# Performance work log

Hardware: AMD Instinct MI355X
Metric: run time of the kernel (lower is better)

## Reference

```python
import jax, jax.numpy as jnp
import numpy as np

NH, DK, DV = 8, 10, 10  # num_heads, per-head key dim, per-head value dim (dim_k=dim_v=80)


def setup_inputs() -> dict:
    key = jax.random.key(0)
    k1, k2, k3, k4, k5 = jax.random.split(key, 5)
    B, NX, NY = 64, 512, 512
    x = jax.random.normal(k1, (B, NX, 768), dtype=jnp.float32)
    y = jax.random.normal(k2, (B, NY, 283), dtype=jnp.float32)
    # nn.Linear(bias=False) weights, stored transposed as (in, out); scaled init
    Wq = jax.random.normal(k3, (768, 80), dtype=jnp.float32) * 0.02
    Wk = jax.random.normal(k4, (283, 80), dtype=jnp.float32) * 0.02
    Wv = jax.random.normal(k5, (283, 80), dtype=jnp.float32) * 0.02
    return {"x": x, "y": y, "Wq": Wq, "Wk": Wk, "Wv": Wv}


def reference(x, y, Wq, Wk, Wv):
    B, nx, _ = x.shape
    ny = y.shape[1]
    # projections -> split heads: (B, nh, seq, dhead)
    q = (x @ Wq).reshape(B, nx, NH, DK).transpose(0, 2, 1, 3)
    k = (y @ Wk).reshape(B, ny, NH, DK).transpose(0, 2, 1, 3)
    v = (y @ Wv).reshape(B, ny, NH, DV).transpose(0, 2, 1, 3)
    scale = 1.0 / np.sqrt(DK).astype(np.float32)
    dist = jax.nn.softmax(jnp.einsum("bhqd,bhkd->bhqk", q, k) * scale, axis=-1)
    att = q + jnp.einsum("bhqk,bhkd->bhqd", dist, v)  # residual add of q
    att = att.transpose(0, 2, 1, 3).reshape(B, nx, NH * DV)
    # module returns `result` = flattened attention (fc/BN stack is dead code)
    return att.reshape(B, -1)
```

## Files before the change

### kernel.cpp

```cpp
#include <hip/hip_runtime.h>
#include <stdint.h>

typedef unsigned short u16;
typedef unsigned int   u32;
typedef _Float16       f16;

typedef __attribute__((ext_vector_type(2))) _Float16 half2v;
typedef __attribute__((ext_vector_type(4))) _Float16 half4v;
typedef __attribute__((ext_vector_type(8))) _Float16 half8v;
typedef __attribute__((ext_vector_type(4))) float    floatx4;

#define NXS    512
#define NYS    512
#define NHEAD  8
#define DHEAD  10
#define DMODEL 80
#define DXK    768
#define DYK    283

__device__ inline half2v pk2(float x, float y) {
  return __builtin_bit_cast(half2v, __builtin_amdgcn_cvt_pkrtz(x, y));
}
__device__ inline half4v cvt4(float4 v) {
  return __builtin_shufflevector(pk2(v.x, v.y), pk2(v.z, v.w), 0, 1, 2, 3);
}

__global__ __launch_bounds__(256) void w_prep(const float* __restrict__ Wq,
                                              const float* __restrict__ Wk,
                                              const float* __restrict__ Wv,
                                              f16* __restrict__ Tq,
                                              f16* __restrict__ Tk,
                                              f16* __restrict__ Tv) {
  const int idx = blockIdx.x * 256 + threadIdx.x;
  if (idx < 80 * 768) {
    const int c = idx / 768, k = idx - c * 768;
    Tq[idx] = (f16)Wq[k * 80 + c];
  }
  if (idx < 80 * 288) {
    const int c = idx / 288, k = idx - c * 288;
    float a = 0.f, b = 0.f;
    if (k < DYK) { a = Wk[k * 80 + c]; b = Wv[k * 80 + c]; }
    Tk[idx] = (f16)a;
    Tv[idx] = (f16)b;
  }
}

__global__ __launch_bounds__(256) void proj_q(const float* __restrict__ X,
                                              const f16* __restrict__ Wt,
                                              f16* __restrict__ O) {
  __shared__ f16 Xs[64 * 40];
  __shared__ f16 Ws[80 * 40];
  const int t = threadIdx.x;
  const int wv = t >> 6, lane = t & 63, m16 = lane & 15, quad = lane >> 4;
  const int row0 = blockIdx.x * 64;
  const int xr_r = t >> 3, xr_k = (t & 7) << 2;
  const int wi0 = t, wi1 = t + 160;

  float4 xr0, xr1;
  uint4 wr0, wr1;
  xr0 = *(const float4*)&X[(size_t)(row0 + xr_r) * DXK + xr_k];
  xr1 = *(const float4*)&X[(size_t)(row0 + xr_r + 32) * DXK + xr_k];
  if (t < 160) {
    wr0 = *(const uint4*)&Wt[(wi0 >> 2) * DXK + (wi0 & 3) * 8];
    wr1 = *(const uint4*)&Wt[(wi1 >> 2) * DXK + (wi1 & 3) * 8];
  }

  floatx4 acc[5];
#pragma unroll
  for (int i = 0; i < 5; ++i) acc[i] = (floatx4){0.f, 0.f, 0.f, 0.f};

  for (int s = 0; s < 24; ++s) {
    if (s) __syncthreads();
    *(half4v*)&Xs[xr_r * 40 + xr_k] = cvt4(xr0);
    *(half4v*)&Xs[(xr_r + 32) * 40 + xr_k] = cvt4(xr1);
    if (t < 160) {
      *(uint4*)&Ws[(wi0 >> 2) * 40 + (wi0 & 3) * 8] = wr0;
      *(uint4*)&Ws[(wi1 >> 2) * 40 + (wi1 & 3) * 8] = wr1;
    }
    __syncthreads();
    if (s < 23) {
      const int k0 = (s + 1) * 32;
      xr0 = *(const float4*)&X[(size_t)(row0 + xr_r) * DXK + k0 + xr_k];
      xr1 = *(const float4*)&X[(size_t)(row0 + xr_r + 32) * DXK + k0 + xr_k];
      if (t < 160) {
        wr0 = *(const uint4*)&Wt[(wi0 >> 2) * DXK + k0 + (wi0 & 3) * 8];
        wr1 = *(const uint4*)&Wt[(wi1 >> 2) * DXK + k0 + (wi1 & 3) * 8];
      }
    }
    const half8v a = *(const half8v*)&Xs[(wv * 16 + m16) * 40 + quad * 8];
#pragma unroll
    for (int nt = 0; nt < 5; ++nt) {
      const half8v b = *(const half8v*)&Ws[(nt * 16 + m16) * 40 + quad * 8];
      acc[nt] = __builtin_amdgcn_mfma_f32_16x16x32_f16(a, b, acc[nt], 0, 0, 0);
    }
  }
#pragma unroll
  for (int nt = 0; nt < 5; ++nt) {
    const int col = nt * 16 + m16;
#pragma unroll
    for (int p = 0; p < 4; ++p) {
      const int grow = row0 + wv * 16 + quad * 4 + p;
      O[(size_t)grow * DMODEL + col] = (f16)acc[nt][p];
    }
  }
}

__global__ __launch_bounds__(256) void proj_kv(const float* __restrict__ Y,
                                               const f16* __restrict__ Wtk,
                                               const f16* __restrict__ Wtv,
                                               f16* __restrict__ Ko,
                                               f16* __restrict__ Vo) {
  __shared__ f16 Ys[64 * 40];
  __shared__ f16 Wks[80 * 40];
  __shared__ f16 Wvs[80 * 40];
  const int t = threadIdx.x;
  const int wv = t >> 6, lane = t & 63, m16 = lane & 15, quad = lane >> 4;
  const int row0 = blockIdx.x * 64;
  const int wi0 = t, wi1 = t + 160;

  float yr[8];
  uint4 wk0, wk1, wv0, wv1;
#pragma unroll
  for (int i = 0; i < 8; ++i) {
    const int idx = t + 256 * i;
    const int r = idx >> 5, kk = idx & 31;
    yr[i] = (kk < DYK) ? Y[(size_t)(row0 + r) * DYK + kk] : 0.f;
  }
  if (t < 160) {
    wk0 = *(const uint4*)&Wtk[(wi0 >> 2) * 288 + (wi0 & 3) * 8];
    wk1 = *(const uint4*)&Wtk[(wi1 >> 2) * 288 + (wi1 & 3) * 8];
    wv0 = *(const uint4*)&Wtv[(wi0 >> 2) * 288 + (wi0 & 3) * 8];
    wv1 = *(const uint4*)&Wtv[(wi1 >> 2) * 288 + (wi1 & 3) * 8];
  }

  floatx4 ak[5], av[5];
#pragma unroll
  for (int i = 0; i < 5; ++i) {
    ak[i] = (floatx4){0.f, 0.f, 0.f, 0.f};
    av[i] = (floatx4){0.f, 0.f, 0.f, 0.f};
  }

  for (int s = 0; s < 9; ++s) {
    if (s) __syncthreads();
#pragma unroll
    for (int i = 0; i < 8; ++i) {
      const int idx = t + 256 * i;
      Ys[(idx >> 5) * 40 + (idx & 31)] = (f16)yr[i];
    }
    if (t < 160) {
      *(uint4*)&Wks[(wi0 >> 2) * 40 + (wi0 & 3) * 8] = wk0;
      *(uint4*)&Wks[(wi1 >> 2) * 40 + (wi1 & 3) * 8] = wk1;
      *(uint4*)&Wvs[(wi0 >> 2) * 40 + (wi0 & 3) * 8] = wv0;
      *(uint4*)&Wvs[(wi1 >> 2) * 40 + (wi1 & 3) * 8] = wv1;
    }
    __syncthreads();
    if (s < 8) {
      const int k0 = (s + 1) * 32;
#pragma unroll
      for (int i = 0; i < 8; ++i) {
        const int idx = t + 256 * i;
        const int r = idx >> 5, k = k0 + (idx & 31);
        yr[i] = (k < DYK) ? Y[(size_t)(row0 + r) * DYK + k] : 0.f;
      }
      if (t < 160) {
        wk0 = *(const uint4*)&Wtk[(wi0 >> 2) * 288 + k0 + (wi0 & 3) * 8];
        wk1 = *(const uint4*)&Wtk[(wi1 >> 2) * 288 + k0 + (wi1 & 3) * 8];
        wv0 = *(const uint4*)&Wtv[(wi0 >> 2) * 288 + k0 + (wi0 & 3) * 8];
        wv1 = *(const uint4*)&Wtv[(wi1 >> 2) * 288 + k0 + (wi1 & 3) * 8];
      }
    }
    const half8v a = *(const half8v*)&Ys[(wv * 16 + m16) * 40 + quad * 8];
#pragma unroll
    for (int nt = 0; nt < 5; ++nt) {
      const half8v bk = *(const half8v*)&Wks[(nt * 16 + m16) * 40 + quad * 8];
      ak[nt] = __builtin_amdgcn_mfma_f32_16x16x32_f16(a, bk, ak[nt], 0, 0, 0);
      const half8v bv = *(const half8v*)&Wvs[(nt * 16 + m16) * 40 + quad * 8];
      av[nt] = __builtin_amdgcn_mfma_f32_16x16x32_f16(a, bv, av[nt], 0, 0, 0);
    }
  }
#pragma unroll
  for (int nt = 0; nt < 5; ++nt) {
    const int col = nt * 16 + m16;
    const int h = col / 10, d = col - h * 10;
#pragma unroll
    for (int p = 0; p < 4; ++p) {
      const int grow = row0 + wv * 16 + quad * 4 + p;
      const int bb = grow >> 9, ny = grow & 511;
      const size_t o = (((size_t)bb * NHEAD + h) * NYS + ny) * DHEAD + d;
      Ko[o] = (f16)ak[nt][p];
      Vo[o] = (f16)av[nt][p];
    }
  }
}

__global__ __launch_bounds__(256) void attn(const f16* __restrict__ Q,
                                            const f16* __restrict__ K,
                                            const f16* __restrict__ V,
                                            float* __restrict__ O) {
  __shared__ f16 Qs[512 * 20];
  __shared__ f16 Ks[512 * 20];
  __shared__ f16 Vt[16 * 520];
  const int t = threadIdx.x;
  const int wv = t >> 6, lane = t & 63, m16 = lane & 15, quad = lane >> 4;
  const int b = blockIdx.x >> 3, h = blockIdx.x & 7;

  u32* Qs32 = (u32*)Qs;
  u32* Ks32 = (u32*)Ks;
  u32* Vt32 = (u32*)Vt;
  const u32* Qg = (const u32*)Q + (size_t)b * NXS * 40 + h * 5;
  const u32* Kg = (const u32*)K + (size_t)(b * NHEAD + h) * NYS * 5;
  const u32* Vg = (const u32*)V + (size_t)(b * NHEAD + h) * NYS * 5;

  for (int idx = t; idx < 2560; idx += 256) {
    const u32 row = (u32)idx / 5u, c = (u32)idx - row * 5u;
    Qs32[row * 10 + c] = Qg[row * 40 + c];
    Ks32[row * 10 + c] = Kg[idx];
    const half2v hv = __builtin_bit_cast(half2v, Vg[idx]);
    Vt[(2 * c) * 520 + row] = hv[0];
    Vt[(2 * c + 1) * 520 + row] = hv[1];
  }
  for (int idx = t; idx < 2560; idx += 256) {
    const u32 row = (u32)idx / 5u, c = 5u + ((u32)idx - row * 5u);
    Qs32[row * 10 + c] = 0u;
    Ks32[row * 10 + c] = 0u;
  }
  for (int idx = t; idx < 1560; idx += 256) {
    Vt32[2600 + idx] = 0u;
  }
  __syncthreads();

  const float scale = 0.31622776601683794f;
#pragma unroll 1
  for (int i = 0; i < 8; ++i) {
    const int qt = wv * 8 + i;
    const half4v qf = *(const half4v*)&Qs[(qt * 16 + m16) * 20 + quad * 4];
    floatx4 oacc = (floatx4){0.f, 0.f, 0.f, 0.f};
    float lp = 0.f;
    for (int kt = 0; kt < 32; ++kt) {
      const half4v kf = *(const half4v*)&Ks[(kt * 16 + m16) * 20 + quad * 4];
      floatx4 s = __builtin_amdgcn_mfma_f32_16x16x16f16(kf, qf,
                    (floatx4){0.f, 0.f, 0.f, 0.f}, 0, 0, 0);
      const float p0 = __expf(s[0] * scale);
      const float p1 = __expf(s[1] * scale);
      const float p2 = __expf(s[2] * scale);
      const float p3 = __expf(s[3] * scale);
      lp += (p0 + p1) + (p2 + p3);
      const half4v pf = __builtin_shufflevector(pk2(p0, p1), pk2(p2, p3), 0, 1, 2, 3);
      const half4v vf = *(const half4v*)&Vt[m16 * 520 + kt * 16 + quad * 4];
      oacc = __builtin_amdgcn_mfma_f32_16x16x16f16(pf, vf, oacc, 0, 0, 0);
    }
    lp += __shfl_xor(lp, 16);
    lp += __shfl_xor(lp, 32);
#pragma unroll
    for (int p = 0; p < 4; ++p) {
      const int rq = qt * 16 + quad * 4 + p;
      const float lr = __shfl(lp, quad * 4 + p);
      const float qv = (float)Qs[rq * 20 + m16];
      const float val = qv + oacc[p] / lr;
      if (m16 < DHEAD)
        O[((size_t)b * NXS + rq) * DMODEL + h * DHEAD + m16] = val;
    }
  }
}

extern "C" void kernel_launch(void* const* d_in, const int* in_sizes, int n_in,
                              void* d_out, int out_size, void* d_ws, size_t ws_size,
                              hipStream_t stream) {
  const float* x  = (const float*)d_in[0];
  const float* y  = (const float*)d_in[1];
  const float* Wq = (const float*)d_in[2];
  const float* Wk = (const float*)d_in[3];
  const float* Wv = (const float*)d_in[4];
  float* out = (float*)d_out;

  char* ws = (char*)d_ws;
  f16* Wtq = (f16*)(ws);
  f16* Wtk = (f16*)(ws + 122880);
  f16* Wtv = (f16*)(ws + 168960);
  f16* Qw  = (f16*)(ws + 262144);
  f16* Kw  = (f16*)(ws + 5505024);
  f16* Vw  = (f16*)(ws + 10747904);

  w_prep <<<240, 256, 0, stream>>>(Wq, Wk, Wv, Wtq, Wtk, Wtv);
  proj_q <<<512, 256, 0, stream>>>(x, Wtq, Qw);
  proj_kv<<<512, 256, 0, stream>>>(y, Wtk, Wtv, Kw, Vw);
  attn   <<<512, 256, 0, stream>>>(Qw, Kw, Vw, out);
}
```

Measured before the change: 238.3 us.

## Merge projection kernels, drop LDS staging, split attention blocks by query half

The Q and K/V projection kernels are merged into one launch of 1024 blocks. Each wave now loads X/Y rows and weight fragments straight from global memory into MFMA operands, with no shared-memory staging and no barriers. The attention kernel is split into two blocks per (batch, head), reads Q fragments directly from global memory, folds the scale into Q, uses padded LDS strides, and keeps two accumulators to split the dependency chain. The trade is more redundant global/L2 traffic for the weights in exchange for more parallelism and fewer syncs, and K/V tiles are now staged twice per head.

```diff
diff --git a/kernel.cpp b/kernel.cpp
--- a/kernel.cpp
+++ b/kernel.cpp
@@ -17,12 +17,17 @@
 #define DMODEL 80
 #define DXK    768
 #define DYK    283
+#define DYKP   288
 
 __device__ inline half2v pk2(float x, float y) {
   return __builtin_bit_cast(half2v, __builtin_amdgcn_cvt_pkrtz(x, y));
 }
 __device__ inline half4v cvt4(float4 v) {
   return __builtin_shufflevector(pk2(v.x, v.y), pk2(v.z, v.w), 0, 1, 2, 3);
+}
+__device__ inline half4v h4u32(u32 a, u32 b) {
+  return __builtin_shufflevector(__builtin_bit_cast(half2v, a),
+                                 __builtin_bit_cast(half2v, b), 0, 1, 2, 3);
 }
 
 __global__ __launch_bounds__(256) void w_prep(const float* __restrict__ Wq,
@@ -45,150 +50,97 @@
   }
 }
 
-__global__ __launch_bounds__(256) void proj_q(const float* __restrict__ X,
-                                              const f16* __restrict__ Wt,
-                                              f16* __restrict__ O) {
-  __shared__ f16 Xs[64 * 40];
-  __shared__ f16 Ws[80 * 40];
+__global__ __launch_bounds__(256) void proj(const float* __restrict__ X,
+                                            const float* __restrict__ Y,
+                                            const f16* __restrict__ Wtq,
+                                            const f16* __restrict__ Wtk,
+                                            const f16* __restrict__ Wtv,
+                                            f16* __restrict__ Qw,
+                                            f16* __restrict__ Kw,
+                                            f16* __restrict__ Vw) {
   const int t = threadIdx.x;
   const int wv = t >> 6, lane = t & 63, m16 = lane & 15, quad = lane >> 4;
-  const int row0 = blockIdx.x * 64;
-  const int xr_r = t >> 3, xr_k = (t & 7) << 2;
-  const int wi0 = t, wi1 = t + 160;
-
-  float4 xr0, xr1;
-  uint4 wr0, wr1;
-  xr0 = *(const float4*)&X[(size_t)(row0 + xr_r) * DXK + xr_k];
-  xr1 = *(const float4*)&X[(size_t)(row0 + xr_r + 32) * DXK + xr_k];
-  if (t < 160) {
-    wr0 = *(const uint4*)&Wt[(wi0 >> 2) * DXK + (wi0 & 3) * 8];
-    wr1 = *(const uint4*)&Wt[(wi1 >> 2) * DXK + (wi1 & 3) * 8];
-  }
-
-  floatx4 acc[5];
-#pragma unroll
-  for (int i = 0; i < 5; ++i) acc[i] = (floatx4){0.f, 0.f, 0.f, 0.f};
-
-  for (int s = 0; s < 24; ++s) {
-    if (s) __syncthreads();
-    *(half4v*)&Xs[xr_r * 40 + xr_k] = cvt4(xr0);
-    *(half4v*)&Xs[(xr_r + 32) * 40 + xr_k] = cvt4(xr1);
-    if (t < 160) {
-      *(uint4*)&Ws[(wi0 >> 2) * 40 + (wi0 & 3) * 8] = wr0;
-      *(uint4*)&Ws[(wi1 >> 2) * 40 + (wi1 & 3) * 8] = wr1;
-    }
-    __syncthreads();
-    if (s < 23) {
-      const int k0 = (s + 1) * 32;
-      xr0 = *(const float4*)&X[(size_t)(row0 + xr_r) * DXK + k0 + xr_k];
-      xr1 = *(const float4*)&X[(size_t)(row0 + xr_r + 32) * DXK + k0 + xr_k];
-      if (t < 160) {
-        wr0 = *(const uint4*)&Wt[(wi0 >> 2) * DXK + k0 + (wi0 & 3) * 8];
-        wr1 = *(const uint4*)&Wt[(wi1 >> 2) * DXK + k0 + (wi1 & 3) * 8];
-      }
-    }
-    const half8v a = *(const half8v*)&Xs[(wv * 16 + m16) * 40 + quad * 8];
+  const int blk = blockIdx.x;
+
+  if (blk < 512) {
+    const int rowb = blk * 64 + wv * 16;
+    const float* xr = X + (size_t)(rowb + m16) * DXK + quad * 8;
+    const f16* wb = Wtq + (size_t)m16 * DXK + quad * 8;
+
+    floatx4 acc[5];
+#pragma unroll
+    for (int i = 0; i < 5; ++i) acc[i] = (floatx4){0.f, 0.f, 0.f, 0.f};
+
+#pragma unroll 4
+    for (int s = 0; s < 24; ++s) {
+      const int k0 = s * 32;
+      const float4 x0 = *(const float4*)(xr + k0);
+      const float4 x1 = *(const float4*)(xr + k0 + 4);
+      const half8v a = __builtin_shufflevector(cvt4(x0), cvt4(x1),
+                                               0, 1, 2, 3, 4, 5, 6, 7);
+#pragma unroll
+      for (int nt = 0; nt < 5; ++nt) {
+        const half8v b = *(const half8v*)(wb + (size_t)nt * 16 * DXK + k0);
+        acc[nt] = __builtin_amdgcn_mfma_f32_16x16x32_f16(a, b, acc[nt], 0, 0, 0);
+      }
+    }
 #pragma unroll
     for (int nt = 0; nt < 5; ++nt) {
-      const half8v b = *(const half8v*)&Ws[(nt * 16 + m16) * 40 + quad * 8];
-      acc[nt] = __builtin_amdgcn_mfma_f32_16x16x32_f16(a, b, acc[nt], 0, 0, 0);
-    }
-  }
-#pragma unroll
-  for (int nt = 0; nt < 5; ++nt) {
-    const int col = nt * 16 + m16;
-#pragma unroll
-    for (int p = 0; p < 4; ++p) {
-      const int grow = row0 + wv * 16 + quad * 4 + p;
-      O[(size_t)grow * DMODEL + col] = (f16)acc[nt][p];
-    }
-  }
-}
-
-__global__ __launch_bounds__(256) void proj_kv(const float* __restrict__ Y,
-                                               const f16* __restrict__ Wtk,
-                                               const f16* __restrict__ Wtv,
-                                               f16* __restrict__ Ko,
-                                               f16* __restrict__ Vo) {
-  __shared__ f16 Ys[64 * 40];
-  __shared__ f16 Wks[80 * 40];
-  __shared__ f16 Wvs[80 * 40];
-  const int t = threadIdx.x;
-  const int wv = t >> 6, lane = t & 63, m16 = lane & 15, quad = lane >> 4;
-  const int row0 = blockIdx.x * 64;
-  const int wi0 = t, wi1 = t + 160;
-
-  float yr[8];
-  uint4 wk0, wk1, wv0, wv1;
-#pragma unroll
-  for (int i = 0; i < 8; ++i) {
-    const int idx = t + 256 * i;
-    const int r = idx >> 5, kk = idx & 31;
-    yr[i] = (kk < DYK) ? Y[(size_t)(row0 + r) * DYK + kk] : 0.f;
-  }
-  if (t < 160) {
-    wk0 = *(const uint4*)&Wtk[(wi0 >> 2) * 288 + (wi0 & 3) * 8];
-    wk1 = *(const uint4*)&Wtk[(wi1 >> 2) * 288 + (wi1 & 3) * 8];
-    wv0 = *(const uint4*)&Wtv[(wi0 >> 2) * 288 + (wi0 & 3) * 8];
-    wv1 = *(const uint4*)&Wtv[(wi1 >> 2) * 288 + (wi1 & 3) * 8];
-  }
-
-  floatx4 ak[5], av[5];
-#pragma unroll
-  for (int i = 0; i < 5; ++i) {
-    ak[i] = (floatx4){0.f, 0.f, 0.f, 0.f};
-    av[i] = (floatx4){0.f, 0.f, 0.f, 0.f};
-  }
-
-  for (int s = 0; s < 9; ++s) {
-    if (s) __syncthreads();
-#pragma unroll
-    for (int i = 0; i < 8; ++i) {
-      const int idx = t + 256 * i;
-      Ys[(idx >> 5) * 40 + (idx & 31)] = (f16)yr[i];
-    }
-    if (t < 160) {
-      *(uint4*)&Wks[(wi0 >> 2) * 40 + (wi0 & 3) * 8] = wk0;
-      *(uint4*)&Wks[(wi1 >> 2) * 40 + (wi1 & 3) * 8] = wk1;
-      *(uint4*)&Wvs[(wi0 >> 2) * 40 + (wi0 & 3) * 8] = wv0;
-      *(uint4*)&Wvs[(wi1 >> 2) * 40 + (wi1 & 3) * 8] = wv1;
-    }
-    __syncthreads();
-    if (s < 8) {
-      const int k0 = (s + 1) * 32;
-#pragma unroll
-      for (int i = 0; i < 8; ++i) {
-        const int idx = t + 256 * i;
-        const int r = idx >> 5, k = k0 + (idx & 31);
-        yr[i] = (k < DYK) ? Y[(size_t)(row0 + r) * DYK + k] : 0.f;
-      }
-      if (t < 160) {
-        wk0 = *(const uint4*)&Wtk[(wi0 >> 2) * 288 + k0 + (wi0 & 3) * 8];
-        wk1 = *(const uint4*)&Wtk[(wi1 >> 2) * 288 + k0 + (wi1 & 3) * 8];
-        wv0 = *(const uint4*)&Wtv[(wi0 >> 2) * 288 + k0 + (wi0 & 3) * 8];
-        wv1 = *(const uint4*)&Wtv[(wi1 >> 2) * 288 + k0 + (wi1 & 3) * 8];
-      }
-    }
-    const half8v a = *(const half8v*)&Ys[(wv * 16 + m16) * 40 + quad * 8];
+      const int col = nt * 16 + m16;
+#pragma unroll
+      for (int p = 0; p < 4; ++p)
+        Qw[(size_t)(rowb + quad * 4 + p) * DMODEL + col] = (f16)acc[nt][p];
+    }
+  } else {
+    const int rowb = (blk - 512) * 64 + wv * 16;
+    const float* yr = Y + (size_t)(rowb + m16) * DYK + quad * 8;
+    const f16* wbk = Wtk + (size_t)m16 * DYKP + quad * 8;
+    const f16* wbv = Wtv + (size_t)m16 * DYKP + quad * 8;
+
+    floatx4 ak[5], av[5];
+#pragma unroll
+    for (int i = 0; i < 5; ++i) {
+      ak[i] = (floatx4){0.f, 0.f, 0.f, 0.f};
+      av[i] = (floatx4){0.f, 0.f, 0.f, 0.f};
+    }
+
+#pragma unroll 2
+    for (int s = 0; s < 9; ++s) {
+      const int k0 = s * 32;
+      float y8[8];
+      if (s < 8) {
+#pragma unroll
+        for (int j = 0; j < 8; ++j) y8[j] = yr[k0 + j];
+      } else {
+#pragma unroll
+        for (int j = 0; j < 8; ++j) {
+          const int k = k0 + quad * 8 + j;
+          y8[j] = (k < DYK) ? yr[k0 + j] : 0.f;
+        }
+      }
+      const half8v a = __builtin_shufflevector(
+          cvt4((float4){y8[0], y8[1], y8[2], y8[3]}),
+          cvt4((float4){y8[4], y8[5], y8[6], y8[7]}), 0, 1, 2, 3, 4, 5, 6, 7);
+#pragma unroll
+      for (int nt = 0; nt < 5; ++nt) {
+        const half8v bk = *(const half8v*)(wbk + (size_t)nt * 16 * DYKP + k0);
+        ak[nt] = __builtin_amdgcn_mfma_f32_16x16x32_f16(a, bk, ak[nt], 0, 0, 0);
+        const half8v bv = *(const half8v*)(wbv + (size_t)nt * 16 * DYKP + k0);
+        av[nt] = __builtin_amdgcn_mfma_f32_16x16x32_f16(a, bv, av[nt], 0, 0, 0);
+      }
+    }
 #pragma unroll
     for (int nt = 0; nt < 5; ++nt) {
-      const half8v bk = *(const half8v*)&Wks[(nt * 16 + m16) * 40 + quad * 8];
-      ak[nt] = __builtin_amdgcn_mfma_f32_16x16x32_f16(a, bk, ak[nt], 0, 0, 0);
-      const half8v bv = *(const half8v*)&Wvs[(nt * 16 + m16) * 40 + quad * 8];
-      av[nt] = __builtin_amdgcn_mfma_f32_16x16x32_f16(a, bv, av[nt], 0, 0, 0);
-    }
-  }
-#pragma unroll
-  for (int nt = 0; nt < 5; ++nt) {
-    const int col = nt * 16 + m16;
-    const int h = col / 10, d = col - h * 10;
-#pragma unroll
-    for (int p = 0; p < 4; ++p) {
-      const int grow = row0 + wv * 16 + quad * 4 + p;
-      const int bb = grow >> 9, ny = grow & 511;
-      const size_t o = (((size_t)bb * NHEAD + h) * NYS + ny) * DHEAD + d;
-      Ko[o] = (f16)ak[nt][p];
-      Vo[o] = (f16)av[nt][p];
+      const int col = nt * 16 + m16;
+      const int h = col / 10, d = col - h * 10;
+#pragma unroll
+      for (int p = 0; p < 4; ++p) {
+        const int grow = rowb + quad * 4 + p;
+        const int bb = grow >> 9, ny = grow & 511;
+        const size_t o = (((size_t)bb * NHEAD + h) * NYS + ny) * DHEAD + d;
+        Kw[o] = (f16)ak[nt][p];
+        Vw[o] = (f16)av[nt][p];
+      }
     }
   }
 }
@@ -197,68 +149,92 @@
                                             const f16* __restrict__ K,
                                             const f16* __restrict__ V,
                                             float* __restrict__ O) {
-  __shared__ f16 Qs[512 * 20];
-  __shared__ f16 Ks[512 * 20];
-  __shared__ f16 Vt[16 * 520];
+  __shared__ f16 Ks[512 * 22];
+  __shared__ f16 Vt[16 * 522];
   const int t = threadIdx.x;
   const int wv = t >> 6, lane = t & 63, m16 = lane & 15, quad = lane >> 4;
-  const int b = blockIdx.x >> 3, h = blockIdx.x & 7;
-
-  u32* Qs32 = (u32*)Qs;
-  u32* Ks32 = (u32*)Ks;
-  u32* Vt32 = (u32*)Vt;
-  const u32* Qg = (const u32*)Q + (size_t)b * NXS * 40 + h * 5;
-  const u32* Kg = (const u32*)K + (size_t)(b * NHEAD + h) * NYS * 5;
-  const u32* Vg = (const u32*)V + (size_t)(b * NHEAD + h) * NYS * 5;
-
+  const int bh = blockIdx.x >> 1, half = blockIdx.x & 1;
+  const int b = bh >> 3, h = bh & 7;
+
+  const u32* Kg = (const u32*)K + (size_t)bh * NYS * 5;
+  const u32* Vg = (const u32*)V + (size_t)bh * NYS * 5;
   for (int idx = t; idx < 2560; idx += 256) {
     const u32 row = (u32)idx / 5u, c = (u32)idx - row * 5u;
-    Qs32[row * 10 + c] = Qg[row * 40 + c];
-    Ks32[row * 10 + c] = Kg[idx];
-    const half2v hv = __builtin_bit_cast(half2v, Vg[idx]);
-    Vt[(2 * c) * 520 + row] = hv[0];
-    Vt[(2 * c + 1) * 520 + row] = hv[1];
-  }
-  for (int idx = t; idx < 2560; idx += 256) {
-    const u32 row = (u32)idx / 5u, c = 5u + ((u32)idx - row * 5u);
-    Qs32[row * 10 + c] = 0u;
-    Ks32[row * 10 + c] = 0u;
-  }
-  for (int idx = t; idx < 1560; idx += 256) {
-    Vt32[2600 + idx] = 0u;
-  }
+    const half2v kv = __builtin_bit_cast(half2v, Kg[idx]);
+    Ks[row * 22 + 2 * c]     = kv[0];
+    Ks[row * 22 + 2 * c + 1] = kv[1];
+    const half2v vv = __builtin_bit_cast(half2v, Vg[idx]);
+    Vt[(2 * c) * 522 + row]     = vv[0];
+    Vt[(2 * c + 1) * 522 + row] = vv[1];
+  }
+  for (int idx = t; idx < 3072; idx += 256) {
+    const u32 row = (u32)idx / 6u, d = 10u + ((u32)idx - row * 6u);
+    Ks[row * 22 + d] = (f16)0.f;
+  }
+  for (int idx = t; idx < 6 * 522; idx += 256)
+    Vt[10 * 522 + idx] = (f16)0.f;
   __syncthreads();
 
   const float scale = 0.31622776601683794f;
 #pragma unroll 1
-  for (int i = 0; i < 8; ++i) {
-    const int qt = wv * 8 + i;
-    const half4v qf = *(const half4v*)&Qs[(qt * 16 + m16) * 20 + quad * 4];
-    floatx4 oacc = (floatx4){0.f, 0.f, 0.f, 0.f};
-    float lp = 0.f;
-    for (int kt = 0; kt < 32; ++kt) {
-      const half4v kf = *(const half4v*)&Ks[(kt * 16 + m16) * 20 + quad * 4];
-      floatx4 s = __builtin_amdgcn_mfma_f32_16x16x16f16(kf, qf,
-                    (floatx4){0.f, 0.f, 0.f, 0.f}, 0, 0, 0);
-      const float p0 = __expf(s[0] * scale);
-      const float p1 = __expf(s[1] * scale);
-      const float p2 = __expf(s[2] * scale);
-      const float p3 = __expf(s[3] * scale);
-      lp += (p0 + p1) + (p2 + p3);
-      const half4v pf = __builtin_shufflevector(pk2(p0, p1), pk2(p2, p3), 0, 1, 2, 3);
-      const half4v vf = *(const half4v*)&Vt[m16 * 520 + kt * 16 + quad * 4];
-      oacc = __builtin_amdgcn_mfma_f32_16x16x16f16(pf, vf, oacc, 0, 0, 0);
-    }
+  for (int i = 0; i < 4; ++i) {
+    const int qt = half * 16 + wv * 4 + i;
+    const int qrow = qt * 16 + m16;
+    const u32* Qg32 = (const u32*)(Q + ((size_t)b * NXS + qrow) * DMODEL + h * DHEAD);
+    float s0 = 0.f, s1 = 0.f, s2 = 0.f, s3 = 0.f;
+    if (quad < 2) {
+      const u32 ua = Qg32[quad * 2], ub = Qg32[quad * 2 + 1];
+      const half2v ha = __builtin_bit_cast(half2v, ua);
+      const half2v hb = __builtin_bit_cast(half2v, ub);
+      s0 = (float)ha[0]; s1 = (float)ha[1]; s2 = (float)hb[0]; s3 = (float)hb[1];
+    } else if (quad == 2) {
+      const u32 ua = Qg32[4];
+      const half2v ha = __builtin_bit_cast(half2v, ua);
+      s0 = (float)ha[0]; s1 = (float)ha[1];
+    }
+    const half4v qf = __builtin_shufflevector(pk2(s0 * scale, s1 * scale),
+                                              pk2(s2 * scale, s3 * scale),
+                                              0, 1, 2, 3);
+    floatx4 o0 = (floatx4){0.f, 0.f, 0.f, 0.f};
+    floatx4 o1 = (floatx4){0.f, 0.f, 0.f, 0.f};
+    float l0 = 0.f, l1 = 0.f;
+    for (int kt = 0; kt < 32; kt += 2) {
+#pragma unroll
+      for (int u = 0; u < 2; ++u) {
+        const int ktu = kt + u;
+        const int kb = (ktu * 16 + m16) * 22 + quad * 4;
+        const half4v kf = h4u32(*(const u32*)&Ks[kb], *(const u32*)&Ks[kb + 2]);
+        const floatx4 s = __builtin_amdgcn_mfma_f32_16x16x16f16(
+            kf, qf, (floatx4){0.f, 0.f, 0.f, 0.f}, 0, 0, 0);
+        const float p0 = __expf(s[0]);
+        const float p1 = __expf(s[1]);
+        const float p2 = __expf(s[2]);
+        const float p3 = __expf(s[3]);
+        const half4v pf = __builtin_shufflevector(pk2(p0, p1), pk2(p2, p3),
+                                                  0, 1, 2, 3);
+        const int vb = m16 * 522 + ktu * 16 + quad * 4;
+        const half4v vf = h4u32(*(const u32*)&Vt[vb], *(const u32*)&Vt[vb + 2]);
+        if (u == 0) {
+          l0 += (p0 + p1) + (p2 + p3);
+          o0 = __builtin_amdgcn_mfma_f32_16x16x16f16(pf, vf, o0, 0, 0, 0);
+        } else {
+          l1 += (p0 + p1) + (p2 + p3);
+          o1 = __builtin_amdgcn_mfma_f32_16x16x16f16(pf, vf, o1, 0, 0, 0);
+        }
+      }
+    }
+    float lp = l0 + l1;
     lp += __shfl_xor(lp, 16);
     lp += __shfl_xor(lp, 32);
 #pragma unroll
     for (int p = 0; p < 4; ++p) {
       const int rq = qt * 16 + quad * 4 + p;
       const float lr = __shfl(lp, quad * 4 + p);
-      const float qv = (float)Qs[rq * 20 + m16];
-      const float val = qv + oacc[p] / lr;
-      if (m16 < DHEAD)
-        O[((size_t)b * NXS + rq) * DMODEL + h * DHEAD + m16] = val;
+      if (m16 < DHEAD) {
+        const float qres = (float)Q[((size_t)b * NXS + rq) * DMODEL + h * DHEAD + m16];
+        O[((size_t)b * NXS + rq) * DMODEL + h * DHEAD + m16] =
+            qres + (o0[p] + o1[p]) / lr;
+      }
     }
   }
 }
@@ -281,8 +257,7 @@
   f16* Kw  = (f16*)(ws + 5505024);
   f16* Vw  = (f16*)(ws + 10747904);
 
-  w_prep <<<240, 256, 0, stream>>>(Wq, Wk, Wv, Wtq, Wtk, Wtv);
-  proj_q <<<512, 256, 0, stream>>>(x, Wtq, Qw);
-  proj_kv<<<512, 256, 0, stream>>>(y, Wtk, Wtv, Kw, Vw);
-  attn   <<<512, 256, 0, stream>>>(Qw, Kw, Vw, out);
-}
+  w_prep<<<240, 256, 0, stream>>>(Wq, Wk, Wv, Wtq, Wtk, Wtv);
+  proj  <<<1024, 256, 0, stream>>>(x, y, Wtq, Wtk, Wtv, Qw, Kw, Vw);
+  attn  <<<1024, 256, 0, stream>>>(Qw, Kw, Vw, out);
+}
```

Result: slower. 265.0 us (+11.2%).
